# Kernel tuning notes

Measured on AMD Instinct MI355X. Metric: run time of the kernel, lower is better.

## Reference

```python
import jax, jax.numpy as jnp
import numpy as np

B, F, D = 32, 4096, 256
ALPHA = 0.001


def setup_inputs() -> dict:
    key = jax.random.key(0)
    ks = jax.random.split(key, 9)
    s = 1.0 / np.sqrt(D)
    return {
        "q": jax.random.normal(ks[0], (B, F, D), dtype=jnp.float32),
        "k": jax.random.normal(ks[1], (B, F, D), dtype=jnp.float32),
        "v": jax.random.normal(ks[2], (B, F, D), dtype=jnp.float32),
        "Wq": jax.random.normal(ks[3], (D, D), dtype=jnp.float32) * s,
        "bq": jax.random.normal(ks[4], (D,), dtype=jnp.float32) * 0.01,
        "Wk": jax.random.normal(ks[5], (D, D), dtype=jnp.float32) * s,
        "bk": jax.random.normal(ks[6], (D,), dtype=jnp.float32) * 0.01,
        "Wv": jax.random.normal(ks[7], (D, D), dtype=jnp.float32) * s,
        "bv": jax.random.normal(ks[8], (D,), dtype=jnp.float32) * 0.01,
    }


def reference(q, k, v, Wq, bq, Wk, bk, Wv, bv):
    # nn.Linear: x @ W.T + b
    queries = q @ Wq.T + bq            # [b, f, d]
    keys = k @ Wk.T + bk               # [b, f, d]
    values = v @ Wv.T + bv             # [b, f, d]
    # batched Gram matrix + ridge term
    key_sym = jnp.einsum("bfd,bfe->bde", keys, keys)          # [b, d, d]
    key_sym = key_sym + ALPHA * jnp.eye(D, dtype=key_sym.dtype)
    key_sym_inv = jnp.linalg.inv(key_sym)                      # [b, d, d]
    kkik = jnp.einsum("bde,bfe->bdf", key_sym_inv, keys)       # [b, d, f]
    kkikv = jnp.einsum("bdf,bfe->bde", kkik, values)           # [b, d, d]
    itn = jax.nn.softmax(kkikv, axis=2)                        # sigma=True; softmax over dim 2
    h = jnp.einsum("bfd,bde->be", queries, itn)                # [b, d]
    return h
```

## Files before the change

kernel.cpp:

```cpp
#include <hip/hip_runtime.h>
#include <math.h>

#define FDIM 4096
#define DDIM 256
#define ALPHA_R 0.001f

typedef __attribute__((ext_vector_type(8))) short short8;
typedef __attribute__((ext_vector_type(4))) float f32x4;

__device__ __forceinline__ unsigned cvt_pk_bf16(float lo_e, float hi_e) {
  unsigned r;
  asm("v_cvt_pk_bf16_f32 %0, %1, %2" : "=v"(r) : "v"(lo_e), "v"(hi_e));
  return r;
}

__global__ void colsum_partial_q(const float* __restrict__ q,
                                 float* __restrict__ part) {
  int chunk = blockIdx.x;
  int b     = blockIdx.y;
  int tid = threadIdx.x;
  int rg = tid >> 6, dq = tid & 63;
  const float* p = q + ((size_t)b * FDIM + chunk * 256 + rg) * DDIM + dq * 4;
  float4 s = make_float4(0.f, 0.f, 0.f, 0.f);
  for (int i = 0; i < 64; ++i) {
    float4 t = *(const float4*)(p + (size_t)i * 4 * DDIM);
    s.x += t.x; s.y += t.y; s.z += t.z; s.w += t.w;
  }
  __shared__ __align__(16) float red[4][64][4];
  *(float4*)&red[rg][dq][0] = s;
  __syncthreads();
  if (rg == 0) {
    float4 a0 = *(float4*)&red[0][dq][0];
    float4 a1 = *(float4*)&red[1][dq][0];
    float4 a2 = *(float4*)&red[2][dq][0];
    float4 a3 = *(float4*)&red[3][dq][0];
    float4 t = make_float4(a0.x + a1.x + a2.x + a3.x, a0.y + a1.y + a2.y + a3.y,
                           a0.z + a1.z + a2.z + a3.z, a0.w + a1.w + a2.w + a3.w);
    *(float4*)(part + ((size_t)chunk * 32 + b) * DDIM + dq * 4) = t;
  }
}

__global__ void colsum_reduce_q(const float* __restrict__ part,
                                float* __restrict__ svec) {
  int b = blockIdx.x; int d = threadIdx.x;
  float s = 0.f;
  for (int c = 0; c < 16; ++c) s += part[((size_t)c * 32 + b) * DDIM + d];
  svec[(size_t)b * DDIM + d] = s;
}

__global__ __launch_bounds__(256) void gram_mfma(const float* __restrict__ kg,
                                                 const float* __restrict__ vg,
                                                 float* __restrict__ G,
                                                 float* __restrict__ svec) {
  int flat = blockIdx.x;
  int xcd = flat & 7, s = flat >> 3;
  int b = xcd * 4 + (s >> 4);
  int tile = s & 15;
  int tm = tile >> 2, tn = tile & 3;
  int mBase = tm * 64, nBase = tn * 64;
  const float* Kb = kg + (size_t)b * FDIM * DDIM;
  const float* Vb = vg + (size_t)b * FDIM * DDIM;

  __shared__ __align__(16) unsigned short Ah[64][40], Al[64][40];
  __shared__ __align__(16) unsigned short Bh[64][40], Bl[64][40];
  __shared__ __align__(16) unsigned short Ch[64][40], Cl[64][40];
  __shared__ float sred[4][68];

  int tid = threadIdx.x;
  int w = tid >> 6, lane = tid & 63;
  int wr = w >> 1, wc = w & 1;
  int lrow = lane & 15;
  int kof = (lane >> 4) * 8;

  const float* pA = Kb + mBase + lane;
  const float* pB = Kb + nBase + lane;
  const float* pC = Vb + nBase + lane;

  bool doK = (tn == 0), doV = (tm == 0);
  float sK = 0.f, sV = 0.f;

  float xa[8], xb[8], xc[8];
  auto loadIter = [&](int it) {
    int f = it * 32 + w * 8;
#pragma unroll
    for (int j = 0; j < 8; ++j) {
      xa[j] = pA[(size_t)(f + j) * DDIM];
      xb[j] = pB[(size_t)(f + j) * DDIM];
      xc[j] = pC[(size_t)(f + j) * DDIM];
    }
  };
  auto stash = [&](const float* x, unsigned short (*H)[40], unsigned short (*L)[40]) {
    unsigned h0 = cvt_pk_bf16(x[0], x[1]);
    unsigned h1 = cvt_pk_bf16(x[2], x[3]);
    unsigned h2 = cvt_pk_bf16(x[4], x[5]);
    unsigned h3 = cvt_pk_bf16(x[6], x[7]);
    unsigned l0 = cvt_pk_bf16(x[0] - __uint_as_float(h0 << 16),
                              x[1] - __uint_as_float(h0 & 0xFFFF0000u));
    unsigned l1 = cvt_pk_bf16(x[2] - __uint_as_float(h1 << 16),
                              x[3] - __uint_as_float(h1 & 0xFFFF0000u));
    unsigned l2 = cvt_pk_bf16(x[4] - __uint_as_float(h2 << 16),
                              x[5] - __uint_as_float(h2 & 0xFFFF0000u));
    unsigned l3 = cvt_pk_bf16(x[6] - __uint_as_float(h3 << 16),
                              x[7] - __uint_as_float(h3 & 0xFFFF0000u));
    *(uint4*)&H[lane][w * 8] = make_uint4(h0, h1, h2, h3);
    *(uint4*)&L[lane][w * 8] = make_uint4(l0, l1, l2, l3);
  };

  f32x4 acc0[2][2], acc1[2][2];
#pragma unroll
  for (int mt = 0; mt < 2; ++mt)
#pragma unroll
    for (int nt = 0; nt < 2; ++nt) {
      acc0[mt][nt] = (f32x4){0.f, 0.f, 0.f, 0.f};
      acc1[mt][nt] = (f32x4){0.f, 0.f, 0.f, 0.f};
    }

  loadIter(0);
  for (int it = 0; it < 128; ++it) {
    __syncthreads();
    stash(xa, Ah, Al);
    stash(xb, Bh, Bl);
    stash(xc, Ch, Cl);
    if (doK) sK += ((xa[0] + xa[1]) + (xa[2] + xa[3])) + ((xa[4] + xa[5]) + (xa[6] + xa[7]));
    if (doV) sV += ((xc[0] + xc[1]) + (xc[2] + xc[3])) + ((xc[4] + xc[5]) + (xc[6] + xc[7]));
    __syncthreads();
    if (it < 127) loadIter(it + 1);

    short8 bh[2], bl[2], ch[2], cl[2];
#pragma unroll
    for (int nt = 0; nt < 2; ++nt) {
      int rB = wc * 32 + nt * 16 + lrow;
      bh[nt] = *(const short8*)&Bh[rB][kof];
      bl[nt] = *(const short8*)&Bl[rB][kof];
      ch[nt] = *(const short8*)&Ch[rB][kof];
      cl[nt] = *(const short8*)&Cl[rB][kof];
    }
    __builtin_amdgcn_s_setprio(1);
#pragma unroll
    for (int mt = 0; mt < 2; ++mt) {
      int rA = wr * 32 + mt * 16 + lrow;
      short8 ah = *(const short8*)&Ah[rA][kof];
      short8 al = *(const short8*)&Al[rA][kof];
#pragma unroll
      for (int nt = 0; nt < 2; ++nt) {
        f32x4 t = acc0[mt][nt];
        t = __builtin_amdgcn_mfma_f32_16x16x32_bf16(ah, bh[nt], t, 0, 0, 0);
        t = __builtin_amdgcn_mfma_f32_16x16x32_bf16(ah, bl[nt], t, 0, 0, 0);
        t = __builtin_amdgcn_mfma_f32_16x16x32_bf16(al, bh[nt], t, 0, 0, 0);
        acc0[mt][nt] = t;
        f32x4 u = acc1[mt][nt];
        u = __builtin_amdgcn_mfma_f32_16x16x32_bf16(ah, ch[nt], u, 0, 0, 0);
        u = __builtin_amdgcn_mfma_f32_16x16x32_bf16(ah, cl[nt], u, 0, 0, 0);
        u = __builtin_amdgcn_mfma_f32_16x16x32_bf16(al, ch[nt], u, 0, 0, 0);
        acc1[mt][nt] = u;
      }
    }
    __builtin_amdgcn_s_setprio(0);
  }

  float* G0 = G + ((size_t)b * 2) * 65536;
  float* G1 = G0 + 65536;
#pragma unroll
  for (int mt = 0; mt < 2; ++mt)
#pragma unroll
    for (int nt = 0; nt < 2; ++nt)
#pragma unroll
      for (int r = 0; r < 4; ++r) {
        int row = mBase + wr * 32 + mt * 16 + (lane >> 4) * 4 + r;
        int col = nBase + wc * 32 + nt * 16 + (lane & 15);
        G0[(size_t)row * DDIM + col] = acc0[mt][nt][r];
        G1[(size_t)row * DDIM + col] = acc1[mt][nt][r];
      }

  if (doK) {
    __syncthreads();
    sred[w][lane] = sK;
    __syncthreads();
    if (tid < 64) {
      float t = sred[0][tid] + sred[1][tid] + sred[2][tid] + sred[3][tid];
      svec[(size_t)1 * 32 * 256 + (size_t)b * 256 + mBase + tid] = t;
    }
  }
  if (doV) {
    __syncthreads();
    sred[w][lane] = sV;
    __syncthreads();
    if (tid < 64) {
      float t = sred[0][tid] + sred[1][tid] + sred[2][tid] + sred[3][tid];
      svec[(size_t)2 * 32 * 256 + (size_t)b * 256 + nBase + tid] = t;
    }
  }
}

__global__ void smallvec(const float* __restrict__ Wq, const float* __restrict__ bq,
                         const float* __restrict__ Wk, const float* __restrict__ Wv,
                         const float* __restrict__ svec, float* __restrict__ uvec) {
  int b = blockIdx.x; int d = threadIdx.x;
  __shared__ float sq[256], sk[256], sv[256];
  sq[d] = svec[((size_t)0 * 32 + b) * DDIM + d];
  sk[d] = svec[((size_t)1 * 32 + b) * DDIM + d];
  sv[d] = svec[((size_t)2 * 32 + b) * DDIM + d];
  __syncthreads();
  float uk = 0.f, uv = 0.f, uq = 0.f;
  for (int j = 0; j < 256; j += 4) {
    float4 wk4 = *(const float4*)(Wk + (size_t)d * DDIM + j);
    float4 wv4 = *(const float4*)(Wv + (size_t)d * DDIM + j);
    float4 wq4 = *(const float4*)(Wq + (size_t)d * DDIM + j);
    uk += wk4.x * sk[j] + wk4.y * sk[j + 1] + wk4.z * sk[j + 2] + wk4.w * sk[j + 3];
    uv += wv4.x * sv[j] + wv4.y * sv[j + 1] + wv4.z * sv[j + 2] + wv4.w * sv[j + 3];
    uq += wq4.x * sq[j] + wq4.y * sq[j + 1] + wq4.z * sq[j + 2] + wq4.w * sq[j + 3];
  }
  uvec[((size_t)0 * 32 + b) * DDIM + d] = uk;
  uvec[((size_t)1 * 32 + b) * DDIM + d] = uv;
  uvec[((size_t)2 * 32 + b) * DDIM + d] = uq + 4096.f * bq[d];
}

__global__ __launch_bounds__(256) void gemm_pass1(const float* __restrict__ Wk,
                                                  const float* __restrict__ G,
                                                  float* __restrict__ T) {
  int tile = blockIdx.x, w = blockIdx.y, b = blockIdx.z;
  int tm = tile >> 2, tn = tile & 3;
  const float* A = Wk;
  const float* B = G + ((size_t)b * 2 + w) * 65536;
  float* C = T + ((size_t)b * 2 + w) * 65536;
  __shared__ __align__(16) float As[16][64];
  __shared__ __align__(16) float Bs[16][64];
  int tid = threadIdx.x;
  int ty = tid >> 4, tx = tid & 15;
  int am = tid & 63, ak4 = tid >> 6;
  int brow = tid >> 4, bcol4 = tid & 15;
  int mBase = tm * 64, nBase = tn * 64;
  float acc[4][4];
#pragma unroll
  for (int i = 0; i < 4; i++)
#pragma unroll
    for (int j = 0; j < 4; j++) acc[i][j] = 0.f;
  for (int k0 = 0; k0 < 256; k0 += 16) {
    float4 a = *(const float4*)(A + (size_t)(mBase + am) * DDIM + k0 + ak4 * 4);
    float4 bb = *(const float4*)(B + (size_t)(k0 + brow) * DDIM + nBase + bcol4 * 4);
    __syncthreads();
    As[ak4 * 4 + 0][am] = a.x; As[ak4 * 4 + 1][am] = a.y;
    As[ak4 * 4 + 2][am] = a.z; As[ak4 * 4 + 3][am] = a.w;
    *(float4*)&Bs[brow][bcol4 * 4] = bb;
    __syncthreads();
#pragma unroll
    for (int kstep = 0; kstep < 16; ++kstep) {
      float4 a4 = *(const float4*)&As[kstep][ty * 4];
      float4 b4 = *(const float4*)&Bs[kstep][tx * 4];
      float av[4] = {a4.x, a4.y, a4.z, a4.w};
      float bvv[4] = {b4.x, b4.y, b4.z, b4.w};
#pragma unroll
      for (int i = 0; i < 4; i++)
#pragma unroll
        for (int j = 0; j < 4; j++)
          acc[i][j] = fmaf(av[i], bvv[j], acc[i][j]);
    }
  }
#pragma unroll
  for (int i = 0; i < 4; i++) {
    float4 o = make_float4(acc[i][0], acc[i][1], acc[i][2], acc[i][3]);
    *(float4*)(C + (size_t)(mBase + ty * 4 + i) * DDIM + nBase + tx * 4) = o;
  }
}

__global__ __launch_bounds__(256) void gemm_pass2(const float* __restrict__ T,
                                                  const float* __restrict__ Wk,
                                                  const float* __restrict__ Wv,
                                                  float* __restrict__ S) {
  int tile = blockIdx.x, w = blockIdx.y, b = blockIdx.z;
  int tm = tile >> 2, tn = tile & 3;
  const float* A = T + ((size_t)b * 2 + w) * 65536;
  const float* W = w ? Wv : Wk;
  float* C = S + ((size_t)b * 2 + w) * 65536;
  __shared__ __align__(16) float As[16][64];
  __shared__ __align__(16) float Bs[16][64];
  int tid = threadIdx.x;
  int ty = tid >> 4, tx = tid & 15;
  int am = tid & 63, ak4 = tid >> 6;
  int mBase = tm * 64, nBase = tn * 64;
  float acc[4][4];
#pragma unroll
  for (int i = 0; i < 4; i++)
#pragma unroll
    for (int j = 0; j < 4; j++) acc[i][j] = 0.f;
  for (int k0 = 0; k0 < 256; k0 += 16) {
    float4 a = *(const float4*)(A + (size_t)(mBase + am) * DDIM + k0 + ak4 * 4);
    float4 bb = *(const float4*)(W + (size_t)(nBase + am) * DDIM + k0 + ak4 * 4);
    __syncthreads();
    As[ak4 * 4 + 0][am] = a.x; As[ak4 * 4 + 1][am] = a.y;
    As[ak4 * 4 + 2][am] = a.z; As[ak4 * 4 + 3][am] = a.w;
    Bs[ak4 * 4 + 0][am] = bb.x; Bs[ak4 * 4 + 1][am] = bb.y;
    Bs[ak4 * 4 + 2][am] = bb.z; Bs[ak4 * 4 + 3][am] = bb.w;
    __syncthreads();
#pragma unroll
    for (int kstep = 0; kstep < 16; ++kstep) {
      float4 a4 = *(const float4*)&As[kstep][ty * 4];
      float4 b4 = *(const float4*)&Bs[kstep][tx * 4];
      float av[4] = {a4.x, a4.y, a4.z, a4.w};
      float bvv[4] = {b4.x, b4.y, b4.z, b4.w};
#pragma unroll
      for (int i = 0; i < 4; i++)
#pragma unroll
        for (int j = 0; j < 4; j++)
          acc[i][j] = fmaf(av[i], bvv[j], acc[i][j]);
    }
  }
#pragma unroll
  for (int i = 0; i < 4; i++) {
    float4 o = make_float4(acc[i][0], acc[i][1], acc[i][2], acc[i][3]);
    *(float4*)(C + (size_t)(mBase + ty * 4 + i) * DDIM + nBase + tx * 4) = o;
  }
}

__global__ void rank1(float* __restrict__ S, const float* __restrict__ uvec,
                      const float* __restrict__ bk, const float* __restrict__ bv) {
  int d = blockIdx.x, w = blockIdx.y, b = blockIdx.z;
  int e = threadIdx.x;
  float* row = S + (((size_t)b * 2 + w) * DDIM + d) * DDIM;
  float ukd = uvec[((size_t)0 * 32 + b) * DDIM + d];
  float bkd = bk[d];
  if (w == 0) {
    float uke = uvec[((size_t)0 * 32 + b) * DDIM + e];
    float add = ukd * bk[e] + bkd * uke + 4096.f * bkd * bk[e] + ((d == e) ? ALPHA_R : 0.f);
    row[e] += add;
  } else {
    float uve = uvec[((size_t)1 * 32 + b) * DDIM + e];
    float add = ukd * bv[e] + bkd * uve + 4096.f * bkd * bv[e];
    row[e] += add;
  }
}

__global__ __launch_bounds__(1024, 4) void gj_factor(float* __restrict__ Sb,
                                                     float* __restrict__ Mtg) {
  int b = blockIdx.x;
  float* A = Sb + (size_t)b * 2 * 65536;
  int tid = threadIdx.x;
  int r = tid >> 2;
  int q = tid & 3;

  __shared__ __align__(16) float Mt[64][264];
  __shared__ __align__(16) float Sst[64][200];
  __shared__ __align__(16) float prow[2][64];
  __shared__ float fac[2][256];

  for (int pg = 0; pg < 4; ++pg) {
    float x[16];
    {
      const float* Ar = A + (size_t)r * 256 + pg * 64 + q * 16;
#pragma unroll
      for (int m = 0; m < 4; ++m) {
        float4 t = *(const float4*)(Ar + m * 4);
        x[m * 4 + 0] = t.x; x[m * 4 + 1] = t.y;
        x[m * 4 + 2] = t.z; x[m * 4 + 3] = t.w;
      }
    }
    if (r == pg * 64) {
      *(float4*)&prow[0][q * 16 + 0]  = make_float4(x[0], x[1], x[2], x[3]);
      *(float4*)&prow[0][q * 16 + 4]  = make_float4(x[4], x[5], x[6], x[7]);
      *(float4*)&prow[0][q * 16 + 8]  = make_float4(x[8], x[9], x[10], x[11]);
      *(float4*)&prow[0][q * 16 + 12] = make_float4(x[12], x[13], x[14], x[15]);
    }
    if (q == 0) fac[0][r] = x[0];
    __syncthreads();

#pragma unroll
    for (int jo = 0; jo < 4; ++jo) {
#pragma unroll
      for (int ji = 0; ji < 16; ++ji) {
        const int j = jo * 16 + ji;
        const int p = pg * 64 + j;
        const int buf = j & 1, nb = buf ^ 1;
        float piv = fac[buf][p];
        float ip = 1.0f / piv;
        float g = fac[buf][r] * ip;
        bool diag = (r == p);
#pragma unroll
        for (int m = 0; m < 16; ++m) {
          float pv = prow[buf][q * 16 + m];
          x[m] = diag ? pv * ip : fmaf(-g, pv, x[m]);
        }
        if (q == jo) x[ji] = diag ? ip : (0.f - g);
        if (j < 63) {
          const int jn = j + 1;
          if (r == pg * 64 + jn) {
            *(float4*)&prow[nb][q * 16 + 0]  = make_float4(x[0], x[1], x[2], x[3]);
            *(float4*)&prow[nb][q * 16 + 4]  = make_float4(x[4], x[5], x[6], x[7]);
            *(float4*)&prow[nb][q * 16 + 8]  = make_float4(x[8], x[9], x[10], x[11]);
            *(float4*)&prow[nb][q * 16 + 12] = make_float4(x[12], x[13], x[14], x[15]);
          }
          if (q == (jn >> 4)) fac[nb][r] = x[jn & 15];
        }
        __syncthreads();
      }
    }
#pragma unroll
    for (int m = 0; m < 16; ++m) Mt[q * 16 + m][r] = x[m];
    __syncthreads();

    {
      int j = tid >> 4, rseg = (tid & 15) * 16;
      float* dst = Mtg + (((size_t)b * 4 + pg) * 64 + j) * 256 + rseg;
#pragma unroll
      for (int m = 0; m < 4; ++m) {
        float4 t = make_float4(Mt[j][rseg + m * 4 + 0], Mt[j][rseg + m * 4 + 1],
                               Mt[j][rseg + m * 4 + 2], Mt[j][rseg + m * 4 + 3]);
        *(float4*)(dst + m * 4) = t;
      }
    }

    int W = (3 - pg) * 64;
    if (W > 0) {
      int c_off = (pg + 1) * 64;
      {
        int cpt = W >> 4;
        int jr = tid >> 4, tc = tid & 15;
        const float* src = A + (size_t)(pg * 64 + jr) * 256 + c_off + tc * cpt;
        for (int m = 0; m < cpt; m += 4) {
          float4 t = *(const float4*)(src + m);
          *(float4*)&Sst[jr][tc * cpt + m] = t;
        }
      }
      __syncthreads();
      int colTiles = W >> 3;
      int rt = tid / colTiles;
      int ctile = tid - rt * colTiles;
      if (rt < 32) {
        int r0 = rt * 8, c0 = ctile * 8;
        float acc[8][8];
#pragma unroll
        for (int i = 0; i < 8; ++i)
#pragma unroll
          for (int j2 = 0; j2 < 8; ++j2) acc[i][j2] = 0.f;
        for (int j = 0; j < 64; ++j) {
          float4 m0 = *(const float4*)&Mt[j][r0];
          float4 m1 = *(const float4*)&Mt[j][r0 + 4];
          float4 s0 = *(const float4*)&Sst[j][c0];
          float4 s1 = *(const float4*)&Sst[j][c0 + 4];
          float mv[8] = {m0.x, m0.y, m0.z, m0.w, m1.x, m1.y, m1.z, m1.w};
          float sv[8] = {s0.x, s0.y, s0.z, s0.w, s1.x, s1.y, s1.z, s1.w};
#pragma unroll
          for (int i = 0; i < 8; ++i)
#pragma unroll
            for (int j2 = 0; j2 < 8; ++j2)
              acc[i][j2] = fmaf(mv[i], sv[j2], acc[i][j2]);
        }
#pragma unroll
        for (int ii = 0; ii < 8; ++ii) {
          int row = r0 + ii;
          bool inPanel = ((row >> 6) == pg);
          float* dst = A + (size_t)row * 256 + c_off + c0;
          float4 o0 = make_float4(acc[ii][0], acc[ii][1], acc[ii][2], acc[ii][3]);
          float4 o1 = make_float4(acc[ii][4], acc[ii][5], acc[ii][6], acc[ii][7]);
          if (!inPanel) {
            float4 a0 = *(const float4*)(dst);
            float4 a1 = *(const float4*)(dst + 4);
            o0.x += a0.x; o0.y += a0.y; o0.z += a0.z; o0.w += a0.w;
            o1.x += a1.x; o1.y += a1.y; o1.z += a1.z; o1.w += a1.w;
          }
          *(float4*)(dst) = o0;
          *(float4*)(dst + 4) = o1;
        }
      }
      __syncthreads();
    }
  }
}

__global__ __launch_bounds__(256) void gj_apply(float* __restrict__ Sb,
                                                const float* __restrict__ Mtg) {
  int blk = blockIdx.x;
  int b = blk >> 3;
  int cbase = (blk & 7) * 32;
  float* Bm = Sb + ((size_t)b * 2 + 1) * 65536;
  int tid = threadIdx.x;
  int rt = tid >> 3;
  int ct = tid & 7;

  __shared__ __align__(16) float Mt[64][260];
  __shared__ __align__(8) float Bp[64][34];

  float4 breg[8];
#pragma unroll
  for (int i = 0; i < 8; ++i)
    breg[i] = *(const float4*)(Bm + (size_t)(rt * 8 + i) * 256 + cbase + ct * 4);

  for (int pg = 0; pg < 4; ++pg) {
    __syncthreads();
    {
      int j = tid >> 2, seg = (tid & 3) * 64;
      const float* src = Mtg + (((size_t)b * 4 + pg) * 64 + j) * 256 + seg;
#pragma unroll
      for (int m = 0; m < 16; ++m) {
        float4 t = *(const float4*)(src + m * 4);
        *(float4*)&Mt[j][seg + m * 4] = t;
      }
    }
    if (rt >= pg * 8 && rt < (pg + 1) * 8) {
#pragma unroll
      for (int i = 0; i < 8; ++i) {
        int j = (rt - pg * 8) * 8 + i;
        *(float2*)&Bp[j][ct * 4]     = make_float2(breg[i].x, breg[i].y);
        *(float2*)&Bp[j][ct * 4 + 2] = make_float2(breg[i].z, breg[i].w);
      }
    }
    __syncthreads();

    float acc[8][4];
#pragma unroll
    for (int i = 0; i < 8; ++i)
#pragma unroll
      for (int c = 0; c < 4; ++c) acc[i][c] = 0.f;
#pragma unroll 4
    for (int j = 0; j < 64; ++j) {
      float4 m0 = *(const float4*)&Mt[j][rt * 8];
      float4 m1 = *(const float4*)&Mt[j][rt * 8 + 4];
      float2 b0 = *(const float2*)&Bp[j][ct * 4];
      float2 b1 = *(const float2*)&Bp[j][ct * 4 + 2];
      float mv[8] = {m0.x, m0.y, m0.z, m0.w, m1.x, m1.y, m1.z, m1.w};
      float bv4[4] = {b0.x, b0.y, b1.x, b1.y};
#pragma unroll
      for (int i = 0; i < 8; ++i)
#pragma unroll
        for (int c = 0; c < 4; ++c)
          acc[i][c] = fmaf(mv[i], bv4[c], acc[i][c]);
    }
    bool inPanel = ((rt >> 3) == pg);
#pragma unroll
    for (int i = 0; i < 8; ++i) {
      if (inPanel) {
        breg[i] = make_float4(acc[i][0], acc[i][1], acc[i][2], acc[i][3]);
      } else {
        breg[i].x += acc[i][0]; breg[i].y += acc[i][1];
        breg[i].z += acc[i][2]; breg[i].w += acc[i][3];
      }
    }
  }

#pragma unroll
  for (int i = 0; i < 8; ++i)
    *(float4*)(Bm + (size_t)(rt * 8 + i) * 256 + cbase + ct * 4) = breg[i];
}

__global__ void rowstats(const float* __restrict__ S, float* __restrict__ stats) {
  int b = blockIdx.x;
  const float* X = S + ((size_t)b * 2 + 1) * 65536;
  int tid = threadIdx.x; int lane = tid & 63; int wv = tid >> 6;
  for (int rr = 0; rr < 64; ++rr) {
    int row = rr * 4 + wv;
    float x0 = X[row * 256 + lane];
    float x1 = X[row * 256 + lane + 64];
    float x2 = X[row * 256 + lane + 128];
    float x3 = X[row * 256 + lane + 192];
    float m = fmaxf(fmaxf(x0, x1), fmaxf(x2, x3));
    for (int o = 32; o > 0; o >>= 1) m = fmaxf(m, __shfl_xor(m, o, 64));
    float s = expf(x0 - m) + expf(x1 - m) + expf(x2 - m) + expf(x3 - m);
    for (int o = 32; o > 0; o >>= 1) s += __shfl_xor(s, o, 64);
    if (lane == 0) {
      stats[((size_t)b * 256 + row) * 2 + 0] = m;
      stats[((size_t)b * 256 + row) * 2 + 1] = s;
    }
  }
}

__global__ void final_h(const float* __restrict__ S, const float* __restrict__ stats,
                        const float* __restrict__ uvec, float* __restrict__ out) {
  int b = blockIdx.x; int e = threadIdx.x;
  const float* X = S + ((size_t)b * 2 + 1) * 65536;
  const float* qs = uvec + ((size_t)2 * 32 + b) * DDIM;
  float acc = 0.f;
  for (int d = 0; d < 256; ++d) {
    float m = stats[((size_t)b * 256 + d) * 2 + 0];
    float s = stats[((size_t)b * 256 + d) * 2 + 1];
    acc += qs[d] * expf(X[d * 256 + e] - m) / s;
  }
  out[(size_t)b * 256 + e] = acc;
}

extern "C" void kernel_launch(void* const* d_in, const int* in_sizes, int n_in,
                              void* d_out, int out_size, void* d_ws, size_t ws_size,
                              hipStream_t stream) {
  const float* q  = (const float*)d_in[0];
  const float* k  = (const float*)d_in[1];
  const float* v  = (const float*)d_in[2];
  const float* Wq = (const float*)d_in[3];
  const float* bq = (const float*)d_in[4];
  const float* Wk = (const float*)d_in[5];
  const float* bk = (const float*)d_in[6];
  const float* Wv = (const float*)d_in[7];
  const float* bv = (const float*)d_in[8];
  float* out = (float*)d_out;

  float* ws   = (float*)d_ws;
  float* Gbuf = ws;
  float* Tbuf = Gbuf + (size_t)32 * 2 * 65536;
  float* Sbuf = Tbuf + (size_t)32 * 2 * 65536;
  float* part = Sbuf + (size_t)32 * 2 * 65536;
  float* svec = part + (size_t)16 * 3 * 32 * 256;
  float* uvec = svec + (size_t)3 * 32 * 256;
  float* stats = uvec + (size_t)3 * 32 * 256;

  colsum_partial_q<<<dim3(16, 32), 256, 0, stream>>>(q, part);
  colsum_reduce_q<<<32, 256, 0, stream>>>(part, svec);
  gram_mfma<<<512, 256, 0, stream>>>(k, v, Gbuf, svec);
  smallvec<<<32, 256, 0, stream>>>(Wq, bq, Wk, Wv, svec, uvec);
  gemm_pass1<<<dim3(16, 2, 32), 256, 0, stream>>>(Wk, Gbuf, Tbuf);
  gemm_pass2<<<dim3(16, 2, 32), 256, 0, stream>>>(Tbuf, Wk, Wv, Sbuf);
  rank1<<<dim3(256, 2, 32), 256, 0, stream>>>(Sbuf, uvec, bk, bv);
  gj_factor<<<32, 1024, 0, stream>>>(Sbuf, Gbuf);
  gj_apply<<<256, 256, 0, stream>>>(Sbuf, Gbuf);
  rowstats<<<32, 256, 0, stream>>>(Sbuf, stats);
  final_h<<<32, 256, 0, stream>>>(Sbuf, stats, uvec, out);
}
```

Before: 574.6 us.

## Fuse small kernels and restructure Gauss-Jordan panel factorization

Folds the q column-sum reduction into smallvec, the rank-1 bias/ridge correction into gemm_pass2's epilogue, and the row statistics and final weighted sum into one softmax_h kernel, cutting launches and global round trips. It also rewrites the gj_factor panel step. One wave now inverts the 64x64 diagonal block in registers with shuffles instead of syncing the whole block per pivot, while the other waves stage the panel into shared memory. A blocked multiply then forms the eliminated panel. This trades many __syncthreads for single-wave serial work and larger register use.

New measurement: 940.3 us. +63.7%, slower.

```diff
diff --git a/kernel.cpp b/kernel.cpp
--- a/kernel.cpp
+++ b/kernel.cpp
@@ -38,14 +38,6 @@
                            a0.z + a1.z + a2.z + a3.z, a0.w + a1.w + a2.w + a3.w);
     *(float4*)(part + ((size_t)chunk * 32 + b) * DDIM + dq * 4) = t;
   }
-}
-
-__global__ void colsum_reduce_q(const float* __restrict__ part,
-                                float* __restrict__ svec) {
-  int b = blockIdx.x; int d = threadIdx.x;
-  float s = 0.f;
-  for (int c = 0; c < 16; ++c) s += part[((size_t)c * 32 + b) * DDIM + d];
-  svec[(size_t)b * DDIM + d] = s;
 }
 
 __global__ __launch_bounds__(256) void gram_mfma(const float* __restrict__ kg,
@@ -194,10 +186,13 @@
 
 __global__ void smallvec(const float* __restrict__ Wq, const float* __restrict__ bq,
                          const float* __restrict__ Wk, const float* __restrict__ Wv,
+                         const float* __restrict__ part,
                          const float* __restrict__ svec, float* __restrict__ uvec) {
   int b = blockIdx.x; int d = threadIdx.x;
   __shared__ float sq[256], sk[256], sv[256];
-  sq[d] = svec[((size_t)0 * 32 + b) * DDIM + d];
+  float sqv = 0.f;
+  for (int c = 0; c < 16; ++c) sqv += part[((size_t)c * 32 + b) * DDIM + d];
+  sq[d] = sqv;
   sk[d] = svec[((size_t)1 * 32 + b) * DDIM + d];
   sv[d] = svec[((size_t)2 * 32 + b) * DDIM + d];
   __syncthreads();
@@ -266,7 +261,10 @@
 __global__ __launch_bounds__(256) void gemm_pass2(const float* __restrict__ T,
                                                   const float* __restrict__ Wk,
                                                   const float* __restrict__ Wv,
-                                                  float* __restrict__ S) {
+                                                  float* __restrict__ S,
+                                                  const float* __restrict__ uvec,
+                                                  const float* __restrict__ bk,
+                                                  const float* __restrict__ bv) {
   int tile = blockIdx.x, w = blockIdx.y, b = blockIdx.z;
   int tm = tile >> 2, tn = tile & 3;
   const float* A = T + ((size_t)b * 2 + w) * 65536;
@@ -305,28 +303,32 @@
           acc[i][j] = fmaf(av[i], bvv[j], acc[i][j]);
     }
   }
+  const float* uk = uvec + ((size_t)0 * 32 + b) * DDIM;
+  const float* uvv = uvec + ((size_t)1 * 32 + b) * DDIM;
+  float ukr[4], bkr[4], ue[4], be[4];
+#pragma unroll
+  for (int i = 0; i < 4; ++i) {
+    int row = mBase + ty * 4 + i;
+    ukr[i] = uk[row]; bkr[i] = bk[row];
+  }
+#pragma unroll
+  for (int j = 0; j < 4; ++j) {
+    int col = nBase + tx * 4 + j;
+    ue[j] = w ? uvv[col] : uk[col];
+    be[j] = w ? bv[col] : bk[col];
+  }
 #pragma unroll
   for (int i = 0; i < 4; i++) {
+    int row = mBase + ty * 4 + i;
+#pragma unroll
+    for (int j = 0; j < 4; j++) {
+      int col = nBase + tx * 4 + j;
+      float add = ukr[i] * be[j] + bkr[i] * ue[j] + 4096.f * bkr[i] * be[j];
+      if (w == 0 && row == col) add += ALPHA_R;
+      acc[i][j] += add;
+    }
     float4 o = make_float4(acc[i][0], acc[i][1], acc[i][2], acc[i][3]);
-    *(float4*)(C + (size_t)(mBase + ty * 4 + i) * DDIM + nBase + tx * 4) = o;
-  }
-}
-
-__global__ void rank1(float* __restrict__ S, const float* __restrict__ uvec,
-                      const float* __restrict__ bk, const float* __restrict__ bv) {
-  int d = blockIdx.x, w = blockIdx.y, b = blockIdx.z;
-  int e = threadIdx.x;
-  float* row = S + (((size_t)b * 2 + w) * DDIM + d) * DDIM;
-  float ukd = uvec[((size_t)0 * 32 + b) * DDIM + d];
-  float bkd = bk[d];
-  if (w == 0) {
-    float uke = uvec[((size_t)0 * 32 + b) * DDIM + e];
-    float add = ukd * bk[e] + bkd * uke + 4096.f * bkd * bk[e] + ((d == e) ? ALPHA_R : 0.f);
-    row[e] += add;
-  } else {
-    float uve = uvec[((size_t)1 * 32 + b) * DDIM + e];
-    float add = ukd * bv[e] + bkd * uve + 4096.f * bkd * bv[e];
-    row[e] += add;
+    *(float4*)(C + (size_t)row * DDIM + nBase + tx * 4) = o;
   }
 }
 
@@ -335,66 +337,94 @@
   int b = blockIdx.x;
   float* A = Sb + (size_t)b * 2 * 65536;
   int tid = threadIdx.x;
-  int r = tid >> 2;
-  int q = tid & 3;
-
+  int w = tid >> 6, lane = tid & 63;
+
+  __shared__ __align__(16) char shraw[64 * 264 * 4];
+  float (*Ap)[264] = (float(*)[264])shraw;
+  float (*Sst)[200] = (float(*)[200])shraw;
   __shared__ __align__(16) float Mt[64][264];
-  __shared__ __align__(16) float Sst[64][200];
-  __shared__ __align__(16) float prow[2][64];
-  __shared__ float fac[2][256];
+  __shared__ __align__(16) float Dls[64][68];
 
   for (int pg = 0; pg < 4; ++pg) {
-    float x[16];
+    int pg64 = pg * 64;
+    if (w == 0) {
+      const float* Ad = A + (size_t)pg64 * 256 + pg64;
+      float e[64];
+#pragma unroll
+      for (int r = 0; r < 64; ++r) e[r] = Ad[(size_t)r * 256 + lane];
+      for (int jo = 0; jo < 4; ++jo) {
+#pragma unroll
+        for (int ji = 0; ji < 16; ++ji) {
+          int jlane = jo * 16 + ji;
+          float piv = __shfl(e[ji], jlane);
+          float ip = 1.0f / piv;
+          float pvc = e[ji];
+          bool isj = (lane == jlane);
+          float wsel = isj ? ip : pvc * ip;
+#pragma unroll
+          for (int r = 0; r < 64; ++r) {
+            if (r == ji) continue;
+            float cr = __shfl(e[r], jlane);
+            float z = isj ? 0.f : e[r];
+            e[r] = fmaf(-cr, wsel, z);
+          }
+          e[ji] = isj ? ip : pvc * ip;
+        }
+        float tmp[16];
+#pragma unroll
+        for (int t = 0; t < 16; ++t) tmp[t] = e[t];
+#pragma unroll
+        for (int r = 0; r < 48; ++r) e[r] = e[r + 16];
+#pragma unroll
+        for (int t = 0; t < 16; ++t) e[48 + t] = tmp[t];
+      }
+#pragma unroll
+      for (int r = 0; r < 64; ++r) Dls[r][lane] = e[r];
+    } else {
+      for (int t = tid - 64; t < 4096; t += 960) {
+        int r = t & 255, kq = t >> 8;
+        float4 v2 = *(const float4*)(A + (size_t)r * 256 + pg64 + kq * 4);
+        Ap[kq * 4 + 0][r] = v2.x; Ap[kq * 4 + 1][r] = v2.y;
+        Ap[kq * 4 + 2][r] = v2.z; Ap[kq * 4 + 3][r] = v2.w;
+      }
+    }
+    __syncthreads();
+
     {
-      const float* Ar = A + (size_t)r * 256 + pg * 64 + q * 16;
-#pragma unroll
-      for (int m = 0; m < 4; ++m) {
-        float4 t = *(const float4*)(Ar + m * 4);
-        x[m * 4 + 0] = t.x; x[m * 4 + 1] = t.y;
-        x[m * 4 + 2] = t.z; x[m * 4 + 3] = t.w;
-      }
-    }
-    if (r == pg * 64) {
-      *(float4*)&prow[0][q * 16 + 0]  = make_float4(x[0], x[1], x[2], x[3]);
-      *(float4*)&prow[0][q * 16 + 4]  = make_float4(x[4], x[5], x[6], x[7]);
-      *(float4*)&prow[0][q * 16 + 8]  = make_float4(x[8], x[9], x[10], x[11]);
-      *(float4*)&prow[0][q * 16 + 12] = make_float4(x[12], x[13], x[14], x[15]);
-    }
-    if (q == 0) fac[0][r] = x[0];
-    __syncthreads();
-
-#pragma unroll
-    for (int jo = 0; jo < 4; ++jo) {
-#pragma unroll
-      for (int ji = 0; ji < 16; ++ji) {
-        const int j = jo * 16 + ji;
-        const int p = pg * 64 + j;
-        const int buf = j & 1, nb = buf ^ 1;
-        float piv = fac[buf][p];
-        float ip = 1.0f / piv;
-        float g = fac[buf][r] * ip;
-        bool diag = (r == p);
-#pragma unroll
-        for (int m = 0; m < 16; ++m) {
-          float pv = prow[buf][q * 16 + m];
-          x[m] = diag ? pv * ip : fmaf(-g, pv, x[m]);
+      int j0 = w * 4;
+      int r0 = lane * 4;
+      float macc[4][4];
+#pragma unroll
+      for (int jj = 0; jj < 4; ++jj)
+#pragma unroll
+        for (int ri = 0; ri < 4; ++ri) macc[jj][ri] = 0.f;
+      for (int k = 0; k < 64; ++k) {
+        float4 d4 = *(const float4*)&Dls[k][j0];
+        float4 a4 = *(const float4*)&Ap[k][r0];
+        float dv[4] = {d4.x, d4.y, d4.z, d4.w};
+        float av[4] = {a4.x, a4.y, a4.z, a4.w};
+#pragma unroll
+        for (int jj = 0; jj < 4; ++jj)
+#pragma unroll
+          for (int ri = 0; ri < 4; ++ri)
+            macc[jj][ri] = fmaf(dv[jj], av[ri], macc[jj][ri]);
+      }
+      bool inPanel = (lane >= pg * 16) && (lane < (pg + 1) * 16);
+      if (inPanel) {
+        int rl = r0 - pg64;
+#pragma unroll
+        for (int jj = 0; jj < 4; ++jj)
+#pragma unroll
+          for (int ri = 0; ri < 4; ++ri)
+            Mt[j0 + jj][r0 + ri] = Dls[rl + ri][j0 + jj];
+      } else {
+#pragma unroll
+        for (int jj = 0; jj < 4; ++jj) {
+          float4 o = make_float4(-macc[jj][0], -macc[jj][1], -macc[jj][2], -macc[jj][3]);
+          *(float4*)&Mt[j0 + jj][r0] = o;
         }
-        if (q == jo) x[ji] = diag ? ip : (0.f - g);
-        if (j < 63) {
-          const int jn = j + 1;
-          if (r == pg * 64 + jn) {
-            *(float4*)&prow[nb][q * 16 + 0]  = make_float4(x[0], x[1], x[2], x[3]);
-            *(float4*)&prow[nb][q * 16 + 4]  = make_float4(x[4], x[5], x[6], x[7]);
-            *(float4*)&prow[nb][q * 16 + 8]  = make_float4(x[8], x[9], x[10], x[11]);
-            *(float4*)&prow[nb][q * 16 + 12] = make_float4(x[12], x[13], x[14], x[15]);
-          }
-          if (q == (jn >> 4)) fac[nb][r] = x[jn & 15];
-        }
-        __syncthreads();
-      }
-    }
-#pragma unroll
-    for (int m = 0; m < 16; ++m) Mt[q * 16 + m][r] = x[m];
+      }
+    }
     __syncthreads();
 
     {
@@ -407,20 +437,19 @@
         *(float4*)(dst + m * 4) = t;
       }
     }
-
     int W = (3 - pg) * 64;
+    int c_off = pg64 + 64;
     if (W > 0) {
-      int c_off = (pg + 1) * 64;
-      {
-        int cpt = W >> 4;
-        int jr = tid >> 4, tc = tid & 15;
-        const float* src = A + (size_t)(pg * 64 + jr) * 256 + c_off + tc * cpt;
-        for (int m = 0; m < cpt; m += 4) {
-          float4 t = *(const float4*)(src + m);
-          *(float4*)&Sst[jr][tc * cpt + m] = t;
-        }
-      }
-      __syncthreads();
+      int W4 = W >> 2;
+      for (int t = tid; t < 64 * W4; t += 1024) {
+        int j = t / W4, cq = t - j * W4;
+        float4 v2 = *(const float4*)(A + (size_t)(pg64 + j) * 256 + c_off + cq * 4);
+        *(float4*)&Sst[j][cq * 4] = v2;
+      }
+    }
+    __syncthreads();
+
+    if (W > 0) {
       int colTiles = W >> 3;
       int rt = tid / colTiles;
       int ctile = tid - rt * colTiles;
@@ -461,8 +490,8 @@
           *(float4*)(dst + 4) = o1;
         }
       }
-      __syncthreads();
-    }
+    }
+    __syncthreads();
   }
 }
 
@@ -541,10 +570,15 @@
     *(float4*)(Bm + (size_t)(rt * 8 + i) * 256 + cbase + ct * 4) = breg[i];
 }
 
-__global__ void rowstats(const float* __restrict__ S, float* __restrict__ stats) {
+__global__ void softmax_h(const float* __restrict__ S,
+                          const float* __restrict__ uvec,
+                          float* __restrict__ out) {
   int b = blockIdx.x;
   const float* X = S + ((size_t)b * 2 + 1) * 65536;
   int tid = threadIdx.x; int lane = tid & 63; int wv = tid >> 6;
+  __shared__ float mrow[256], qos[256];
+  __shared__ float qs_s[256];
+  qs_s[tid] = uvec[((size_t)2 * 32 + b) * DDIM + tid];
   for (int rr = 0; rr < 64; ++rr) {
     int row = rr * 4 + wv;
     float x0 = X[row * 256 + lane];
@@ -556,23 +590,17 @@
     float s = expf(x0 - m) + expf(x1 - m) + expf(x2 - m) + expf(x3 - m);
     for (int o = 32; o > 0; o >>= 1) s += __shfl_xor(s, o, 64);
     if (lane == 0) {
-      stats[((size_t)b * 256 + row) * 2 + 0] = m;
-      stats[((size_t)b * 256 + row) * 2 + 1] = s;
-    }
-  }
-}
-
-__global__ void final_h(const float* __restrict__ S, const float* __restrict__ stats,
-                        const float* __restrict__ uvec, float* __restrict__ out) {
-  int b = blockIdx.x; int e = threadIdx.x;
-  const float* X = S + ((size_t)b * 2 + 1) * 65536;
-  const float* qs = uvec + ((size_t)2 * 32 + b) * DDIM;
+      mrow[row] = m;
+      qos[row] = s;
+    }
+  }
+  __syncthreads();
+  qos[tid] = qs_s[tid] / qos[tid];
+  __syncthreads();
+  int e = tid;
   float acc = 0.f;
-  for (int d = 0; d < 256; ++d) {
-    float m = stats[((size_t)b * 256 + d) * 2 + 0];
-    float s = stats[((size_t)b * 256 + d) * 2 + 1];
-    acc += qs[d] * expf(X[d * 256 + e] - m) / s;
-  }
+  for (int d = 0; d < 256; ++d)
+    acc += qos[d] * expf(X[d * 256 + e] - mrow[d]);
   out[(size_t)b * 256 + e] = acc;
 }
 
@@ -597,17 +625,13 @@
   float* part = Sbuf + (size_t)32 * 2 * 65536;
   float* svec = part + (size_t)16 * 3 * 32 * 256;
   float* uvec = svec + (size_t)3 * 32 * 256;
-  float* stats = uvec + (size_t)3 * 32 * 256;
 
   colsum_partial_q<<<dim3(16, 32), 256, 0, stream>>>(q, part);
-  colsum_reduce_q<<<32, 256, 0, stream>>>(part, svec);
   gram_mfma<<<512, 256, 0, stream>>>(k, v, Gbuf, svec);
-  smallvec<<<32, 256, 0, stream>>>(Wq, bq, Wk, Wv, svec, uvec);
+  smallvec<<<32, 256, 0, stream>>>(Wq, bq, Wk, Wv, part, svec, uvec);
   gemm_pass1<<<dim3(16, 2, 32), 256, 0, stream>>>(Wk, Gbuf, Tbuf);
-  gemm_pass2<<<dim3(16, 2, 32), 256, 0, stream>>>(Tbuf, Wk, Wv, Sbuf);
-  rank1<<<dim3(256, 2, 32), 256, 0, stream>>>(Sbuf, uvec, bk, bv);
+  gemm_pass2<<<dim3(16, 2, 32), 256, 0, stream>>>(Tbuf, Wk, Wv, Sbuf, uvec, bk, bv);
   gj_factor<<<32, 1024, 0, stream>>>(Sbuf, Gbuf);
   gj_apply<<<256, 256, 0, stream>>>(Sbuf, Gbuf);
-  rowstats<<<32, 256, 0, stream>>>(Sbuf, stats);
-  final_h<<<32, 256, 0, stream>>>(Sbuf, stats, uvec, out);
-}
+  softmax_h<<<32, 256, 0, stream>>>(Sbuf, uvec, out);
+}
```
